# Performance work log

Measured on AMD Instinct MI355X. Metric: run time of the kernel, lower is better.

The kernel has to match this reference:

```python
import jax, jax.numpy as jnp
import numpy as np
from jax import lax

T, B, D_IN, H = 512, 128, 512, 512


def setup_inputs() -> dict:
    key = jax.random.key(0)
    k1, k2, k3, k4 = jax.random.split(key, 4)
    ins = jax.random.normal(k1, (T, B, D_IN), dtype=jnp.float32)
    resets = jax.random.bernoulli(k2, 0.05, (T, B))  # episode-boundary reset mask
    carry = jnp.zeros((B, H), dtype=jnp.float32)
    # fused GRU weights: gate order (r, z, n); input denses have no bias in flax GRUCell
    Wi = jax.random.normal(k3, (D_IN, 3 * H), dtype=jnp.float32) * (1.0 / np.sqrt(D_IN))
    Wh = jax.random.normal(k4, (H, 3 * H), dtype=jnp.float32) * (1.0 / np.sqrt(H))
    bh = jnp.zeros((3 * H,), dtype=jnp.float32)
    return {"carry": carry, "ins": ins, "resets": resets, "Wi": Wi, "Wh": Wh, "bh": bh}


def reference(carry, ins, resets, Wi, Wh, bh):
    """ScannedRNN forward: scan a flax GRUCell over time with per-step reset masking.

    Returns (final_carry [B,H], ys [T,B,H]).
    """

    def step(h, xr):
        x, r_mask = xr                       # x: [B,D_in], r_mask: [B]
        h = jnp.where(r_mask[:, None], jnp.zeros_like(h), h)
        gi = x @ Wi                          # [B,3H]  (no input bias in flax GRUCell)
        gh = h @ Wh + bh                     # [B,3H]
        ir, iz, inn = jnp.split(gi, 3, axis=-1)
        hr, hz, hn = jnp.split(gh, 3, axis=-1)
        r = jax.nn.sigmoid(ir + hr)
        z = jax.nn.sigmoid(iz + hz)
        n = jnp.tanh(inn + r * hn)
        new_h = (1.0 - z) * n + z * h
        return new_h, new_h                  # GRUCell returns (new_carry, new_carry)

    final_carry, ys = lax.scan(step, carry, (ins, resets))
    return final_carry, ys
```

## Files before the change

### kernel.cpp

```cpp
#include <hip/hip_runtime.h>

#define T_STEPS 512
#define BATCH   128
#define DIN     512
#define HDIM    512
#define THREEH  1536
#define THREADS 256
#define LDK     520
#define LDG     49
#define NGROUP  4
#define NSLICE  32
#define BC      32
#define HC      16
#define NC      48
#define CNT_STRIDE 16
#define SPIN_MAX (1 << 16)
#define EX_DWORDS (NSLICE * BATCH * HC / 2)
#define RW5 16
#define EXSLOT 131072
#define FLAGS_OFF  0
#define GBAR_OFF   1024
#define NONCE_OFF  1536
#define DEC_OFF    1664
#define VD_OFF     2048
#define HS_OFF     3072
#define EX_OFF     4096
#define GI_OFF     (1u<<20)
#define GI_BYTES   201326592ULL

typedef _Float16 half8 __attribute__((ext_vector_type(8)));
typedef _Float16 half4v __attribute__((ext_vector_type(4)));
typedef float    f32x4 __attribute__((ext_vector_type(4)));
typedef unsigned int uint4v __attribute__((ext_vector_type(4)));

__global__ void sniff_kernel(const unsigned int* __restrict__ w,
                             unsigned int* __restrict__ dec) {
  unsigned int local = 0;
  for (int i = threadIdx.x; i < (T_STEPS * BATCH) / 4; i += THREADS) {
    if (w[i] > 1u) local = 1u;
  }
  if (local) atomicOr(dec, 1u);
}

__device__ __forceinline__ void run_gemm(const _Float16* __restrict__ sAa,
                                         const _Float16* __restrict__ sW,
                                         float* __restrict__ sAcc,
                                         int wid, int lane) {
  const int fr = lane & 15;
  const int kb = (lane >> 4) * 8;
  for (int tile = wid; tile < 6; tile += 4) {
    int mi = tile / 3, ni = tile - mi * 3;
    const _Float16* ap = sAa + (mi * 16 + fr) * LDK + kb;
    const _Float16* bp = sW  + (ni * 16 + fr) * LDK + kb;
    f32x4 acc = {0.f, 0.f, 0.f, 0.f};
#pragma unroll
    for (int kk = 0; kk < DIN / 32; ++kk)
      acc = __builtin_amdgcn_mfma_f32_16x16x32_f16(
          *(const half8*)(ap + kk * 32),
          *(const half8*)(bp + kk * 32), acc, 0, 0, 0);
    int crow = mi * 16 + (lane >> 4) * 4;
    int ccol = ni * 16 + fr;
#pragma unroll
    for (int j = 0; j < 4; ++j) sAcc[(crow + j) * LDG + ccol] = acc[j];
  }
}

__global__ __launch_bounds__(THREADS, 1)
void gru_kernel_v1(const float* __restrict__ carry,
                   const float* __restrict__ ins,
                   const void*  __restrict__ resets_raw,
                   const float* __restrict__ Wi,
                   const float* __restrict__ Wh,
                   const float* __restrict__ bh,
                   float* __restrict__ out,
                   unsigned int* __restrict__ cnt,
                   unsigned int* __restrict__ ex0,
                   unsigned int* __restrict__ ex1,
                   const unsigned int* __restrict__ dec)
{
  __shared__ alignas(16) _Float16 sWi[NC * LDK];
  __shared__ alignas(16) _Float16 sWh[NC * LDK];
  __shared__ alignas(16) _Float16 sA [BC * LDK];
  __shared__ float sGi[BC * LDG];
  __shared__ float sGh[BC * LDG];
  __shared__ float sBh[NC];
  __shared__ int   sRst[BC];

  const int tid  = threadIdx.x;
  const int bid  = blockIdx.x;
  const int g    = bid & (NGROUP - 1);
  const int p    = bid >> 2;
  const int row0 = g * BC;
  const int col0 = p * HC;

  float* carryOut = out;
  float* ys = out + BATCH * HDIM;

  const unsigned int isBool = *dec;
  const unsigned char* r8  = (const unsigned char*)resets_raw;
  const int*           r32 = (const int*)resets_raw;

  unsigned int* ex[2] = { ex0, ex1 };
  unsigned int* myCnt = cnt + g * CNT_STRIDE;

  for (int idx = tid; idx < DIN * NC; idx += THREADS) {
    int k  = idx / NC;
    int ci = idx - k * NC;
    int gcol = (ci >> 4) * HDIM + col0 + (ci & 15);
    sWi[ci * LDK + k] = (_Float16)Wi[k * THREEH + gcol];
    sWh[ci * LDK + k] = (_Float16)Wh[k * THREEH + gcol];
  }
  if (tid < NC) {
    int gcol = (tid >> 4) * HDIM + col0 + (tid & 15);
    sBh[tid] = bh[gcol];
  }

  float hreg[2];
  {
    int idx = tid * 2;
    int b0 = idx >> 4, c0 = idx & 15;
    hreg[0] = carry[(size_t)(row0 + b0) * HDIM + col0 + c0];
    hreg[1] = carry[(size_t)(row0 + b0) * HDIM + col0 + c0 + 1];
  }

  const int wid  = tid >> 6;
  const int lane = tid & 63;

  auto stageRst = [&](int t) {
    if (tid < BC) {
      int off = t * BATCH + row0 + tid;
      sRst[tid] = isBool ? (int)r8[off] : r32[off];
    }
  };
  auto stageX = [&](int t) {
    const float4* src = (const float4*)(ins + (size_t)(t * BATCH + row0) * DIN);
    for (int i = tid; i < BC * (DIN / 4); i += THREADS) {
      int r = i >> 7, c4 = i & 127;
      float4 v = src[(size_t)r * 128 + c4];
      half4v hv = {(_Float16)v.x, (_Float16)v.y, (_Float16)v.z, (_Float16)v.w};
      *(half4v*)&sA[r * LDK + c4 * 4] = hv;
    }
  };

  stageRst(0);
  stageX(0);
  __syncthreads();
  run_gemm(sA, sWi, sGi, wid, lane);
  __syncthreads();
  {
    const float4* src = (const float4*)(carry + (size_t)row0 * HDIM);
    for (int i = tid; i < BC * (HDIM / 4); i += THREADS) {
      int r = i >> 7, c4 = i & 127;
      float4 v = src[(size_t)r * 128 + c4];
      float m = sRst[r] ? 0.f : 1.f;
      half4v hv = {(_Float16)(v.x*m), (_Float16)(v.y*m),
                   (_Float16)(v.z*m), (_Float16)(v.w*m)};
      *(half4v*)&sA[r * LDK + c4 * 4] = hv;
    }
  }
  __syncthreads();

  for (int t = 0; t < T_STEPS; ++t) {
    if (t > 0) {
      {
        const unsigned int target = 32u * (unsigned)t;
        unsigned int fv;
        for (int it = 0; it < SPIN_MAX; ++it) {
          asm volatile("global_load_dword %0, %1, off sc0 sc1\n\t"
                       "s_waitcnt vmcnt(0)"
                       : "=v"(fv) : "v"(myCnt) : "memory");
          if (fv >= target) break;
          __builtin_amdgcn_s_sleep(1);
        }
      }
      {
        const unsigned int* exsrc = ex[(t - 1) & 1];
        uint4v vv[8];
#pragma unroll
        for (int j = 0; j < 8; ++j) {
          int i = tid + THREADS * j;
          int p_ = i >> 6, b_ = (i >> 1) & 31, hw = (i & 1) << 2;
          const unsigned int* sp = exsrc + p_ * 1024 + (row0 + b_) * 8 + hw;
          asm volatile("global_load_dwordx4 %0, %1, off sc0 sc1"
                       : "=&v"(vv[j]) : "v"(sp) : "memory");
        }
        asm volatile("s_waitcnt vmcnt(0)" ::: "memory");
        __builtin_amdgcn_sched_barrier(0);
#pragma unroll
        for (int j = 0; j < 8; ++j) {
          int i = tid + THREADS * j;
          int p_ = i >> 6, b_ = (i >> 1) & 31, hw = (i & 1) << 3;
          half8 hv = *reinterpret_cast<half8*>(&vv[j]);
          half8 z = {(_Float16)0, (_Float16)0, (_Float16)0, (_Float16)0,
                     (_Float16)0, (_Float16)0, (_Float16)0, (_Float16)0};
          hv = sRst[b_] ? z : hv;
          *(half8*)&sA[b_ * LDK + p_ * 16 + hw] = hv;
        }
      }
      __syncthreads();
    }

    run_gemm(sA, sWh, sGh, wid, lane);
    __syncthreads();

    {
#pragma unroll
      for (int e = 0; e < 2; ++e) {
        int idx = tid * 2 + e;
        int b = idx >> 4, cj = idx & 15;
        float gir = sGi[b * LDG + cj];
        float giz = sGi[b * LDG + 16 + cj];
        float gin = sGi[b * LDG + 32 + cj];
        float ghr = sGh[b * LDG + cj]      + sBh[cj];
        float ghz = sGh[b * LDG + 16 + cj] + sBh[16 + cj];
        float ghn = sGh[b * LDG + 32 + cj] + sBh[32 + cj];
        float r = 1.f / (1.f + __expf(-(gir + ghr)));
        float z = 1.f / (1.f + __expf(-(giz + ghz)));
        float n = tanhf(gin + r * ghn);
        float hp = sRst[b] ? 0.f : hreg[e];
        hreg[e] = (1.f - z) * n + z * hp;
      }
      union { _Float16 h[2]; unsigned int u; } pk;
      pk.h[0] = (_Float16)hreg[0];
      pk.h[1] = (_Float16)hreg[1];
      unsigned int* dst = ex[t & 1] + p * 1024 + (row0 + (tid >> 3)) * 8 + (tid & 7);
      asm volatile("global_store_dword %0, %1, off sc0 sc1"
                   :: "v"(dst), "v"(pk.u) : "memory");
      int b0 = (tid * 2) >> 4, c0 = (tid * 2) & 15;
      float2 yv = make_float2(hreg[0], hreg[1]);
      *(float2*)&ys[((size_t)t * BATCH + row0 + b0) * HDIM + col0 + c0] = yv;
      if (t == T_STEPS - 1)
        *(float2*)&carryOut[(size_t)(row0 + b0) * HDIM + col0 + c0] = yv;
    }
    asm volatile("s_waitcnt vmcnt(0)" ::: "memory");
    __syncthreads();
    if (tid == 0) atomicAdd(myCnt, 1u);

    if (t < T_STEPS - 1) {
      stageRst(t + 1);
      stageX(t + 1);
      __syncthreads();
      run_gemm(sA, sWi, sGi, wid, lane);
      __syncthreads();
    }
  }
}

__global__ __launch_bounds__(256, 1)
void gi_prepass2(const float* __restrict__ ins,
                 const float* __restrict__ Wi,
                 _Float16* __restrict__ gis)
{
  __shared__ alignas(16) _Float16 sWiT[48 * LDK];
  __shared__ alignas(16) _Float16 sX[32 * LDK];

  const int tid = threadIdx.x;
  const int bid = blockIdx.x;
  const int n   = bid >> 3;
  const int mg  = bid & 7;
  const int wid = tid >> 6;
  const int lane = tid & 63;
  const int fr = lane & 15;
  const int kb = (lane >> 4) * 8;

  for (int idx = tid; idx < 48 * DIN; idx += 256) {
    int ci = idx % 48, k = idx / 48;
    int gcol = (ci >> 4) * HDIM + n * 16 + (ci & 15);
    sWiT[ci * LDK + k] = (_Float16)Wi[(size_t)k * THREEH + gcol];
  }

  float4 va[16];
  auto LOADS = [&](int ch) {
    const float4* src = (const float4*)(ins + (size_t)(mg * 8192 + ch * 32) * DIN);
#pragma unroll
    for (int j = 0; j < 16; ++j) va[j] = src[tid + 256 * j];
  };
  auto WRITE = [&]() {
#pragma unroll
    for (int j = 0; j < 16; ++j) {
      int i = tid + 256 * j;
      int r = i >> 7, c4 = i & 127;
      float4 v = va[j];
      half4v hv = {(_Float16)v.x, (_Float16)v.y, (_Float16)v.z, (_Float16)v.w};
      *(half4v*)&sX[r * LDK + c4 * 4] = hv;
    }
  };

  LOADS(0);
  for (int ch = 0; ch < 256; ++ch) {
    WRITE();
    __syncthreads();
    if (ch + 1 < 256) LOADS(ch + 1);

    const int m0 = mg * 8192 + ch * 32;
    const int tt = m0 >> 7;
    const int bb0 = m0 & 127;
    for (int tile = wid; tile < 6; tile += 4) {
      int mi = tile / 3, ni = tile - mi * 3;
      const _Float16* ap = sX   + (mi * 16 + fr) * LDK + kb;
      const _Float16* bp = sWiT + (ni * 16 + fr) * LDK + kb;
      f32x4 acc = {0.f, 0.f, 0.f, 0.f};
#pragma unroll
      for (int kk = 0; kk < DIN / 32; ++kk)
        acc = __builtin_amdgcn_mfma_f32_16x16x32_f16(
            *(const half8*)(ap + kk * 32),
            *(const half8*)(bp + kk * 32), acc, 0, 0, 0);
      int gr = mi * 16 + ((lane >> 4) << 2);
      int col = n * 16 + fr;
      size_t base = ((size_t)(tt * 3 + ni) * BATCH) * HDIM + col;
#pragma unroll
      for (int j = 0; j < 4; ++j)
        gis[base + (size_t)(bb0 + gr + j) * HDIM] = (_Float16)acc[j];
    }
    __syncthreads();
  }
}

__device__ __forceinline__ void gridbar(unsigned int* ctr, int tid) {
  __syncthreads();
  if (tid == 0) {
    atomicAdd(ctr, 1u);
    unsigned int v;
    for (int it = 0; it < SPIN_MAX; ++it) {
      asm volatile("global_load_dword %0, %1, off sc0 sc1\n\t"
                   "s_waitcnt vmcnt(0)" : "=v"(v) : "v"(ctr) : "memory");
      if (v >= 256u) break;
      __builtin_amdgcn_s_sleep(1);
    }
  }
  __syncthreads();
}

__global__ __launch_bounds__(256, 1)
void gru_kernel_v5(const float* __restrict__ carry,
                   const void*  __restrict__ resets_raw,
                   const float* __restrict__ Wh,
                   const float* __restrict__ bh,
                   float* __restrict__ out,
                   unsigned int* __restrict__ wsb,
                   const _Float16* __restrict__ gis,
                   const unsigned int* __restrict__ dec)
{
  __shared__ alignas(16) _Float16 sWh[NC * LDK];
  __shared__ alignas(16) _Float16 sA [RW5 * LDK];
  __shared__ float sGh[RW5 * LDG];
  __shared__ alignas(16) _Float16 sGi[2 * 3 * 16 * 16];
  __shared__ float sBh[NC];
  __shared__ char  sRstAll[T_STEPS * RW5];
  __shared__ int   sFast;
  __shared__ unsigned int sNonce;

  const int tid  = threadIdx.x;
  const int bid  = blockIdx.x;
  const int g    = bid & 7;
  const int p    = bid >> 3;
  const int row0 = g * RW5;
  const int col0 = p * HC;

  unsigned int* flags    = wsb + (FLAGS_OFF / 4);
  unsigned int* gbars    = wsb + (GBAR_OFF / 4);
  unsigned int* nonceArr = wsb + (NONCE_OFF / 4);
  unsigned int* vd       = wsb + (VD_OFF / 4);
  unsigned int* hs       = wsb + (HS_OFF / 4);
  char*         exb      = (char*)wsb + EX_OFF;

  float* carryOut = out;
  float* ys = out + BATCH * HDIM;

  const unsigned int isBool = *dec;
  const unsigned char* r8  = (const unsigned char*)resets_raw;
  const int*           r32 = (const int*)resets_raw;
  const unsigned short* gisu = (const unsigned short*)gis;

  const int wid  = tid >> 6;
  const int lane = tid & 63;
  const int fr   = lane & 15;
  const int kb   = (lane >> 4) * 8;
  const int gb   = tid >> 4;
  const int gc   = tid & 15;

  for (int idx = tid; idx < DIN * NC; idx += THREADS) {
    int k  = idx / NC;
    int ci = idx - k * NC;
    int gcol = (ci >> 4) * HDIM + col0 + (ci & 15);
    sWh[ci * LDK + k] = (_Float16)Wh[k * THREEH + gcol];
  }
  if (tid < NC) {
    int gcol = (tid >> 4) * HDIM + col0 + (tid & 15);
    sBh[tid] = bh[gcol];
  }
  for (int idx = tid; idx < T_STEPS * RW5; idx += THREADS) {
    int tt = idx >> 4, r = idx & 15;
    int off = tt * BATCH + row0 + r;
    sRstAll[idx] = isBool ? (char)(r8[off] != 0) : (char)(r32[off] != 0);
  }
  float hreg = carry[(size_t)(row0 + gb) * HDIM + col0 + gc];

  if (p == 0 && tid == 0) {
    unsigned long long tv = __builtin_amdgcn_s_memrealtime();
    unsigned int nv = (unsigned int)(tv ^ (tv >> 32));
    if (nv == 0) nv = 0x5A5A5A5Au;
    unsigned int* np = nonceArr + g;
    asm volatile("global_store_dword %0, %1, off sc0 sc1\n\t"
                 "s_waitcnt vmcnt(0)" :: "v"(np), "v"(nv) : "memory");
  }
  gridbar(gbars + 0 * 16, tid);
  if (tid == 0) {
    unsigned int nv;
    asm volatile("global_load_dword %0, %1, off sc0 sc1\n\t"
                 "s_waitcnt vmcnt(0)" : "=v"(nv) : "v"(nonceArr + g) : "memory");
    sNonce = nv;
  }
  __syncthreads();
  const unsigned int nonce = sNonce;

  bool okAll = true;
  for (int r = 0; r < 2; ++r) {
    gridbar(gbars + (1 + r) * 16, tid);
    if (tid == 0) {
      unsigned int tok = nonce ^ ((unsigned)p << 8) ^ ((unsigned)(r + 1) << 20);
      asm volatile("global_store_dword %0, %1, off sc0\n\t"
                   "s_waitcnt vmcnt(0)" :: "v"(hs + bid), "v"(tok) : "memory");
    }
    __syncthreads();
    for (int s = 0; s < 40; ++s) __builtin_amdgcn_s_sleep(2);
    if (tid < 32) {
      unsigned int v;
      const unsigned int* hp = hs + (g + 8 * tid);
      asm volatile("global_load_dword %0, %1, off sc0\n\t"
                   "s_waitcnt vmcnt(0)" : "=v"(v) : "v"(hp) : "memory");
      unsigned int expv = nonce ^ ((unsigned)tid << 8) ^ ((unsigned)(r + 1) << 20);
      okAll = okAll && (v == expv);
    }
  }
  {
    bool wgok = __all((tid < 32) ? okAll : true);
    if (tid == 0) {
      unsigned int vv = wgok ? 1u : 0u;
      asm volatile("global_store_dword %0, %1, off sc0 sc1\n\t"
                   "s_waitcnt vmcnt(0)" :: "v"(vd + bid), "v"(vv) : "memory");
    }
    gridbar(gbars + 3 * 16, tid);
    bool fin = true;
    if (tid < 32) {
      unsigned int v;
      asm volatile("global_load_dword %0, %1, off sc0 sc1\n\t"
                   "s_waitcnt vmcnt(0)" : "=v"(v) : "v"(vd + (g + 8 * tid)) : "memory");
      fin = (v == 1u);
    }
    bool unan = __all((tid < 32) ? fin : true);
    if (tid == 0) sFast = unan ? 1 : 0;
    __syncthreads();
  }
  const int fast = sFast;

  if (tid == 0) {
    unsigned int* fp = flags + (g * 32 + p);
    unsigned int zz = 0u;
    if (fast) asm volatile("global_store_dword %0, %1, off sc0\n\ts_waitcnt vmcnt(0)" :: "v"(fp), "v"(zz) : "memory");
    else      asm volatile("global_store_dword %0, %1, off sc0 sc1\n\ts_waitcnt vmcnt(0)" :: "v"(fp), "v"(zz) : "memory");
  }
  {
    union { _Float16 h; unsigned short u; } ck;
    ck.h = (_Float16)hreg;
    unsigned int cv = (unsigned int)ck.u;
    char* cdst = exb + EXSLOT + g * 16384 + gb * 1024 + (col0 + gc) * 2;
    if (fast) asm volatile("global_store_short %0, %1, off sc0" :: "v"(cdst), "v"(cv) : "memory");
    else      asm volatile("global_store_short %0, %1, off sc0 sc1" :: "v"(cdst), "v"(cv) : "memory");
    asm volatile("s_waitcnt vmcnt(0)" ::: "memory");
  }
  gridbar(gbars + 4 * 16, tid);

  {
    size_t base = ((size_t)0 * BATCH + row0 + gb) * HDIM + col0 + gc;
    unsigned short v0 = gisu[base];
    unsigned short v1 = gisu[base + (size_t)BATCH * HDIM];
    unsigned short v2 = gisu[base + 2 * (size_t)BATCH * HDIM];
    union { unsigned short u; _Float16 h; } c;
    c.u = v0; sGi[(0 * 16 + gb) * 16 + gc] = c.h;
    c.u = v1; sGi[(1 * 16 + gb) * 16 + gc] = c.h;
    c.u = v2; sGi[(2 * 16 + gb) * 16 + gc] = c.h;
  }
  uint4v w3a = {0, 0, 0, 0}, w3b = {0, 0, 0, 0};
  if (fast && wid == 3 && lane < 48) {
    int gamma = lane >> 4, row = lane & 15;
    const char* sp = (const char*)(gisu + ((size_t)(1 * 3 + gamma) * BATCH + row0 + row) * HDIM + col0);
    asm volatile("global_load_dwordx4 %0, %2, off\n\t"
                 "global_load_dwordx4 %1, %2, off offset:16"
                 : "=v"(w3a), "=v"(w3b) : "v"(sp) : "memory");
  }
  __syncthreads();

  for (int t = 0; t < T_STEPS; ++t) {
    const int slot = t & 1;
    if (fast) {
      if (t > 0) {
        unsigned int fv = 0xFFFFFFFFu;
        const unsigned int* fp = flags + g * 32 + (tid & 31);
        bool done = false;
        for (int it = 0; it < SPIN_MAX && !done; ++it) {
          if (tid < 32)
            asm volatile("global_load_dword %0, %1, off sc0\n\t"
                         "s_waitcnt vmcnt(0)" : "=v"(fv) : "v"(fp) : "memory");
          done = __all((tid < 32) ? (fv >= (unsigned)t) : true);
          if (!done && it > 256) __builtin_amdgcn_s_sleep(1);
        }
      }
      __syncthreads();

      if (wid < 3) {
        const char* abase = exb + (slot ^ 1) * EXSLOT + g * 16384 + fr * 1024 + kb * 2;
        uint4v af[16];
#pragma unroll
        for (int kk = 0; kk < 16; ++kk) {
          const char* sp = abase + kk * 64;
          asm volatile("global_load_dwordx4 %0, %1, off sc0"
                       : "=v"(af[kk]) : "v"(sp) : "memory");
        }
        asm volatile("s_waitcnt vmcnt(0)" ::: "memory");
        __builtin_amdgcn_sched_barrier(0);
        int rr = (int)sRstAll[t * 16 + fr];
        if (rr) {
#pragma unroll
          for (int kk = 0; kk < 16; ++kk) af[kk] = (uint4v){0, 0, 0, 0};
        }
        const _Float16* bp = sWh + (wid * 16 + fr) * LDK + kb;
        f32x4 a0 = {0.f, 0.f, 0.f, 0.f}, a1 = {0.f, 0.f, 0.f, 0.f};
#pragma unroll
        for (int kk = 0; kk < 16; kk += 2) {
          a0 = __builtin_amdgcn_mfma_f32_16x16x32_f16(
              *(half8*)&af[kk], *(const half8*)(bp + kk * 32), a0, 0, 0, 0);
          a1 = __builtin_amdgcn_mfma_f32_16x16x32_f16(
              *(half8*)&af[kk + 1], *(const half8*)(bp + (kk + 1) * 32), a1, 0, 0, 0);
        }
        a0 += a1;
        int crow = (lane >> 4) * 4;
        int ccol = wid * 16 + fr;
#pragma unroll
        for (int j = 0; j < 4; ++j) sGh[(crow + j) * LDG + ccol] = a0[j];
      } else {
        asm volatile("s_waitcnt vmcnt(0)" ::: "memory");
        __builtin_amdgcn_sched_barrier(0);
        if (lane < 48) {
          int gamma = lane >> 4, row = lane & 15;
          _Float16* d = &sGi[((t + 1) & 1) * 768 + (gamma * 16 + row) * 16];
          *(uint4v*)d = w3a;
          *(uint4v*)(d + 8) = w3b;
        }
        int tn = (t + 2 < T_STEPS) ? t + 2 : T_STEPS - 1;
        if (lane < 48) {
          int gamma = lane >> 4, row = lane & 15;
          const char* sp = (const char*)(gisu + ((size_t)(tn * 3 + gamma) * BATCH + row0 + row) * HDIM + col0);
          asm volatile("global_load_dwordx4 %0, %2, off\n\t"
                       "global_load_dwordx4 %1, %2, off offset:16"
                       : "=v"(w3a), "=v"(w3b) : "v"(sp) : "memory");
        }
      }
      __syncthreads();

      {
        float gir = (float)sGi[slot * 768 + (0 * 16 + gb) * 16 + gc];
        float giz = (float)sGi[slot * 768 + (1 * 16 + gb) * 16 + gc];
        float gin = (float)sGi[slot * 768 + (2 * 16 + gb) * 16 + gc];
        float ghr = sGh[gb * LDG + gc]      + sBh[gc];
        float ghz = sGh[gb * LDG + 16 + gc] + sBh[16 + gc];
        float ghn = sGh[gb * LDG + 32 + gc] + sBh[32 + gc];
        float r = 1.f / (1.f + __expf(-(gir + ghr)));
        float z = 1.f / (1.f + __expf(-(giz + ghz)));
        float n = tanhf(gin + r * ghn);
        float hp = sRstAll[t * 16 + gb] ? 0.f : hreg;
        hreg = (1.f - z) * n + z * hp;
        if (t < T_STEPS - 1) {
          union { _Float16 h; unsigned short u; } pk;
          pk.h = (_Float16)hreg;
          unsigned int pv = (unsigned int)pk.u;
          char* dst = exb + slot * EXSLOT + g * 16384 + gb * 1024 + (col0 + gc) * 2;
          asm volatile("global_store_short %0, %1, off sc0"
                       :: "v"(dst), "v"(pv) : "memory");
        }
      }
      asm volatile("s_waitcnt vmcnt(0)" ::: "memory");
      __syncthreads();
      if (tid == 0 && t < T_STEPS - 1) {
        unsigned int* fp = flags + (g * 32 + p);
        unsigned int val = (unsigned)(t + 1);
        asm volatile("global_store_dword %0, %1, off sc0"
                     :: "v"(fp), "v"(val) : "memory");
      }
      ys[((size_t)t * BATCH + row0 + gb) * HDIM + col0 + gc] = hreg;
      if (t == T_STEPS - 1)
        carryOut[(size_t)(row0 + gb) * HDIM + col0 + gc] = hreg;
    } else {
      unsigned short fg0, fg1, fg2;
      {
        size_t base = ((size_t)(t * 3) * BATCH + row0 + gb) * HDIM + col0 + gc;
        fg0 = gisu[base];
        fg1 = gisu[base + (size_t)BATCH * HDIM];
        fg2 = gisu[base + 2 * (size_t)BATCH * HDIM];
      }
      if (t > 0) {
        unsigned int fv = 0xFFFFFFFFu;
        const unsigned int* fp = flags + g * 32 + (tid & 31);
        bool done = false;
        for (int it = 0; it < SPIN_MAX && !done; ++it) {
          if (tid < 32)
            asm volatile("global_load_dword %0, %1, off sc0 sc1\n\t"
                         "s_waitcnt vmcnt(0)" : "=v"(fv) : "v"(fp) : "memory");
          done = __all((tid < 32) ? (fv >= (unsigned)t) : true);
          if (!done) __builtin_amdgcn_s_sleep(1);
        }
      }
      __syncthreads();

      {
        const char* src = exb + (slot ^ 1) * EXSLOT + g * 16384
                        + (tid >> 4) * 1024 + (tid & 15) * 64;
        uint4v v0, v1, v2, v3;
        asm volatile("global_load_dwordx4 %0, %4, off sc0 sc1\n\t"
                     "global_load_dwordx4 %1, %4, off offset:16 sc0 sc1\n\t"
                     "global_load_dwordx4 %2, %4, off offset:32 sc0 sc1\n\t"
                     "global_load_dwordx4 %3, %4, off offset:48 sc0 sc1\n\t"
                     "s_waitcnt vmcnt(0)"
                     : "=&v"(v0), "=&v"(v1), "=&v"(v2), "=&v"(v3)
                     : "v"(src) : "memory");
        __builtin_amdgcn_sched_barrier(0);
        int r = tid >> 4, c0 = (tid & 15) * 32;
        half8 h0 = *reinterpret_cast<half8*>(&v0);
        half8 h1 = *reinterpret_cast<half8*>(&v1);
        half8 h2 = *reinterpret_cast<half8*>(&v2);
        half8 h3 = *reinterpret_cast<half8*>(&v3);
        half8 z = {(_Float16)0, (_Float16)0, (_Float16)0, (_Float16)0,
                   (_Float16)0, (_Float16)0, (_Float16)0, (_Float16)0};
        if (sRstAll[t * 16 + r]) { h0 = z; h1 = z; h2 = z; h3 = z; }
        *(half8*)&sA[r * LDK + c0 +  0] = h0;
        *(half8*)&sA[r * LDK + c0 +  8] = h1;
        *(half8*)&sA[r * LDK + c0 + 16] = h2;
        *(half8*)&sA[r * LDK + c0 + 24] = h3;
      }
      __syncthreads();

      if (wid < 3) {
        const _Float16* ap = sA  + fr * LDK + kb;
        const _Float16* bp = sWh + (wid * 16 + fr) * LDK + kb;
        f32x4 a0 = {0.f, 0.f, 0.f, 0.f}, a1 = {0.f, 0.f, 0.f, 0.f};
#pragma unroll
        for (int kk = 0; kk < 16; kk += 2) {
          a0 = __builtin_amdgcn_mfma_f32_16x16x32_f16(
              *(const half8*)(ap + kk * 32), *(const half8*)(bp + kk * 32), a0, 0, 0, 0);
          a1 = __builtin_amdgcn_mfma_f32_16x16x32_f16(
              *(const half8*)(ap + (kk + 1) * 32), *(const half8*)(bp + (kk + 1) * 32), a1, 0, 0, 0);
        }
        a0 += a1;
        int crow = (lane >> 4) * 4;
        int ccol = wid * 16 + fr;
#pragma unroll
        for (int j = 0; j < 4; ++j) sGh[(crow + j) * LDG + ccol] = a0[j];
      }
      __syncthreads();

      {
        union { unsigned short u; _Float16 h; } c0_, c1_, c2_;
        c0_.u = fg0; c1_.u = fg1; c2_.u = fg2;
        float gir = (float)c0_.h;
        float giz = (float)c1_.h;
        float gin = (float)c2_.h;
        float ghr = sGh[gb * LDG + gc]      + sBh[gc];
        float ghz = sGh[gb * LDG + 16 + gc] + sBh[16 + gc];
        float ghn = sGh[gb * LDG + 32 + gc] + sBh[32 + gc];
        float r = 1.f / (1.f + __expf(-(gir + ghr)));
        float z = 1.f / (1.f + __expf(-(giz + ghz)));
        float n = tanhf(gin + r * ghn);
        float hp = sRstAll[t * 16 + gb] ? 0.f : hreg;
        hreg = (1.f - z) * n + z * hp;
        if (t < T_STEPS - 1) {
          union { _Float16 h; unsigned short u; } pk;
          pk.h = (_Float16)hreg;
          unsigned int pv = (unsigned int)pk.u;
          char* dst = exb + slot * EXSLOT + g * 16384 + gb * 1024 + (col0 + gc) * 2;
          asm volatile("global_store_short %0, %1, off sc0 sc1"
                       :: "v"(dst), "v"(pv) : "memory");
        }
      }
      asm volatile("s_waitcnt vmcnt(0)" ::: "memory");
      __syncthreads();
      if (tid == 0 && t < T_STEPS - 1) {
        unsigned int* fp = flags + (g * 32 + p);
        unsigned int val = (unsigned)(t + 1);
        asm volatile("global_store_dword %0, %1, off sc0 sc1"
                     :: "v"(fp), "v"(val) : "memory");
      }
      ys[((size_t)t * BATCH + row0 + gb) * HDIM + col0 + gc] = hreg;
      if (t == T_STEPS - 1)
        carryOut[(size_t)(row0 + gb) * HDIM + col0 + gc] = hreg;
    }
  }

  __builtin_amdgcn_fence(__ATOMIC_RELEASE, "agent");
}

extern "C" void kernel_launch(void* const* d_in, const int* in_sizes, int n_in,
                              void* d_out, int out_size, void* d_ws, size_t ws_size,
                              hipStream_t stream) {
  const float* carry  = (const float*)d_in[0];
  const float* ins    = (const float*)d_in[1];
  const void*  resets = (const void*)d_in[2];
  const float* Wi     = (const float*)d_in[3];
  const float* Wh     = (const float*)d_in[4];
  const float* bh     = (const float*)d_in[5];
  float* out = (float*)d_out;

  unsigned int* wsb  = (unsigned int*)d_ws;
  unsigned int* dec  = (unsigned int*)((char*)d_ws + DEC_OFF);
  unsigned int* ex0  = (unsigned int*)((char*)d_ws + EX_OFF);
  unsigned int* ex1  = ex0 + EX_DWORDS;
  _Float16*     gis  = (_Float16*)((char*)d_ws + GI_OFF);

  (void)hipMemsetAsync(d_ws, 0, 4096, stream);

  sniff_kernel<<<dim3(1), dim3(THREADS), 0, stream>>>(
      (const unsigned int*)resets, dec);

  const bool bigWs = ws_size >= (size_t)GI_OFF + GI_BYTES;

  if (bigWs) {
    gi_prepass2<<<dim3(256), dim3(256), 0, stream>>>(ins, Wi, gis);
    void* args[] = { (void*)&carry, (void*)&resets, (void*)&Wh, (void*)&bh,
                     (void*)&out, (void*)&wsb, (void*)&gis, (void*)&dec };
    (void)hipLaunchCooperativeKernel((const void*)gru_kernel_v5,
                                     dim3(256), dim3(256),
                                     args, 0, stream);
  } else {
    void* args[] = { (void*)&carry, (void*)&ins, (void*)&resets, (void*)&Wi,
                     (void*)&Wh, (void*)&bh, (void*)&out, (void*)&wsb,
                     (void*)&ex0, (void*)&ex1, (void*)&dec };
    (void)hipLaunchCooperativeKernel((const void*)gru_kernel_v1,
                                     dim3(NGROUP * NSLICE), dim3(THREADS),
                                     args, 0, stream);
  }
}
```

Before: 2.273 ms.

## Tag exchanged hidden state with step number to replace flag polling

The hidden-state exchange buffer now stores each fp16 value in a dword with the step number in the upper 16 bits. Consumers spin directly on the data until every tag matches, instead of first polling per-block flags and then loading. The per-step flag wait moves to the otherwise idle wave 3 and only guards buffer reuse. Merging the fast and slow paths and replacing fixed sleeps in the handshake with spin loops are meant to shorten the critical path of each recurrent step, at the cost of doubling exchange traffic and a larger workspace memset.

```diff
diff --git a/kernel.cpp b/kernel.cpp
--- a/kernel.cpp
+++ b/kernel.cpp
@@ -15,9 +15,10 @@
 #define NC      48
 #define CNT_STRIDE 16
 #define SPIN_MAX (1 << 16)
+#define HS_SPIN  512
 #define EX_DWORDS (NSLICE * BATCH * HC / 2)
-#define RW5 16
-#define EXSLOT 131072
+#define RW6 16
+#define SLOTSZ 262144
 #define FLAGS_OFF  0
 #define GBAR_OFF   1024
 #define NONCE_OFF  1536
@@ -332,7 +333,7 @@
 }
 
 __global__ __launch_bounds__(256, 1)
-void gru_kernel_v5(const float* __restrict__ carry,
+void gru_kernel_v6(const float* __restrict__ carry,
                    const void*  __restrict__ resets_raw,
                    const float* __restrict__ Wh,
                    const float* __restrict__ bh,
@@ -342,11 +343,11 @@
                    const unsigned int* __restrict__ dec)
 {
   __shared__ alignas(16) _Float16 sWh[NC * LDK];
-  __shared__ alignas(16) _Float16 sA [RW5 * LDK];
-  __shared__ float sGh[RW5 * LDG];
+  __shared__ alignas(16) _Float16 sA [RW6 * LDK];
+  __shared__ float sGh[RW6 * LDG];
   __shared__ alignas(16) _Float16 sGi[2 * 3 * 16 * 16];
   __shared__ float sBh[NC];
-  __shared__ char  sRstAll[T_STEPS * RW5];
+  __shared__ char  sRstAll[T_STEPS * RW6];
   __shared__ int   sFast;
   __shared__ unsigned int sNonce;
 
@@ -354,7 +355,7 @@
   const int bid  = blockIdx.x;
   const int g    = bid & 7;
   const int p    = bid >> 3;
-  const int row0 = g * RW5;
+  const int row0 = g * RW6;
   const int col0 = p * HC;
 
   unsigned int* flags    = wsb + (FLAGS_OFF / 4);
@@ -389,7 +390,7 @@
     int gcol = (tid >> 4) * HDIM + col0 + (tid & 15);
     sBh[tid] = bh[gcol];
   }
-  for (int idx = tid; idx < T_STEPS * RW5; idx += THREADS) {
+  for (int idx = tid; idx < T_STEPS * RW6; idx += THREADS) {
     int tt = idx >> 4, r = idx & 15;
     int off = tt * BATCH + row0 + r;
     sRstAll[idx] = isBool ? (char)(r8[off] != 0) : (char)(r32[off] != 0);
@@ -400,9 +401,8 @@
     unsigned long long tv = __builtin_amdgcn_s_memrealtime();
     unsigned int nv = (unsigned int)(tv ^ (tv >> 32));
     if (nv == 0) nv = 0x5A5A5A5Au;
-    unsigned int* np = nonceArr + g;
     asm volatile("global_store_dword %0, %1, off sc0 sc1\n\t"
-                 "s_waitcnt vmcnt(0)" :: "v"(np), "v"(nv) : "memory");
+                 "s_waitcnt vmcnt(0)" :: "v"(nonceArr + g), "v"(nv) : "memory");
   }
   gridbar(gbars + 0 * 16, tid);
   if (tid == 0) {
@@ -416,22 +416,25 @@
 
   bool okAll = true;
   for (int r = 0; r < 2; ++r) {
-    gridbar(gbars + (1 + r) * 16, tid);
     if (tid == 0) {
       unsigned int tok = nonce ^ ((unsigned)p << 8) ^ ((unsigned)(r + 1) << 20);
       asm volatile("global_store_dword %0, %1, off sc0\n\t"
                    "s_waitcnt vmcnt(0)" :: "v"(hs + bid), "v"(tok) : "memory");
     }
     __syncthreads();
-    for (int s = 0; s < 40; ++s) __builtin_amdgcn_s_sleep(2);
     if (tid < 32) {
-      unsigned int v;
+      unsigned int expv = nonce ^ ((unsigned)tid << 8) ^ ((unsigned)(r + 1) << 20);
       const unsigned int* hp = hs + (g + 8 * tid);
-      asm volatile("global_load_dword %0, %1, off sc0\n\t"
-                   "s_waitcnt vmcnt(0)" : "=v"(v) : "v"(hp) : "memory");
-      unsigned int expv = nonce ^ ((unsigned)tid << 8) ^ ((unsigned)(r + 1) << 20);
-      okAll = okAll && (v == expv);
-    }
+      bool got = false;
+      for (int it = 0; it < HS_SPIN && !got; ++it) {
+        unsigned int v;
+        asm volatile("global_load_dword %0, %1, off sc0\n\t"
+                     "s_waitcnt vmcnt(0)" : "=v"(v) : "v"(hp) : "memory");
+        got = (v == expv);
+      }
+      okAll = okAll && got;
+    }
+    gridbar(gbars + (1 + r) * 16, tid);
   }
   {
     bool wgok = __all((tid < 32) ? okAll : true);
@@ -454,99 +457,122 @@
   }
   const int fast = sFast;
 
-  if (tid == 0) {
-    unsigned int* fp = flags + (g * 32 + p);
-    unsigned int zz = 0u;
-    if (fast) asm volatile("global_store_dword %0, %1, off sc0\n\ts_waitcnt vmcnt(0)" :: "v"(fp), "v"(zz) : "memory");
-    else      asm volatile("global_store_dword %0, %1, off sc0 sc1\n\ts_waitcnt vmcnt(0)" :: "v"(fp), "v"(zz) : "memory");
-  }
   {
     union { _Float16 h; unsigned short u; } ck;
     ck.h = (_Float16)hreg;
-    unsigned int cv = (unsigned int)ck.u;
-    char* cdst = exb + EXSLOT + g * 16384 + gb * 1024 + (col0 + gc) * 2;
-    if (fast) asm volatile("global_store_short %0, %1, off sc0" :: "v"(cdst), "v"(cv) : "memory");
-    else      asm volatile("global_store_short %0, %1, off sc0 sc1" :: "v"(cdst), "v"(cv) : "memory");
+    unsigned int cv = (1u << 16) | (unsigned int)ck.u;
+    char* cdst = exb + 1 * SLOTSZ + g * 32768 + ((gb * 512) + (col0 + gc)) * 4;
+    if (fast) asm volatile("global_store_dword %0, %1, off sc0" :: "v"(cdst), "v"(cv) : "memory");
+    else      asm volatile("global_store_dword %0, %1, off sc0 sc1" :: "v"(cdst), "v"(cv) : "memory");
     asm volatile("s_waitcnt vmcnt(0)" ::: "memory");
   }
-  gridbar(gbars + 4 * 16, tid);
 
   {
     size_t base = ((size_t)0 * BATCH + row0 + gb) * HDIM + col0 + gc;
-    unsigned short v0 = gisu[base];
-    unsigned short v1 = gisu[base + (size_t)BATCH * HDIM];
-    unsigned short v2 = gisu[base + 2 * (size_t)BATCH * HDIM];
     union { unsigned short u; _Float16 h; } c;
-    c.u = v0; sGi[(0 * 16 + gb) * 16 + gc] = c.h;
-    c.u = v1; sGi[(1 * 16 + gb) * 16 + gc] = c.h;
-    c.u = v2; sGi[(2 * 16 + gb) * 16 + gc] = c.h;
+    c.u = gisu[base];                              sGi[(0 * 16 + gb) * 16 + gc] = c.h;
+    c.u = gisu[base + (size_t)BATCH * HDIM];       sGi[(1 * 16 + gb) * 16 + gc] = c.h;
+    c.u = gisu[base + 2 * (size_t)BATCH * HDIM];   sGi[(2 * 16 + gb) * 16 + gc] = c.h;
   }
   uint4v w3a = {0, 0, 0, 0}, w3b = {0, 0, 0, 0};
-  if (fast && wid == 3 && lane < 48) {
+  if (wid == 3 && lane < 48) {
     int gamma = lane >> 4, row = lane & 15;
-    const char* sp = (const char*)(gisu + ((size_t)(1 * 3 + gamma) * BATCH + row0 + row) * HDIM + col0);
+    const char* sp = (const char*)(gisu + ((size_t)(3 + gamma) * BATCH + row0 + row) * HDIM + col0);
     asm volatile("global_load_dwordx4 %0, %2, off\n\t"
                  "global_load_dwordx4 %1, %2, off offset:16"
                  : "=v"(w3a), "=v"(w3b) : "v"(sp) : "memory");
   }
   __syncthreads();
 
+  const int srow = tid >> 4;
+  const int sc0_ = (tid & 15) * 32;
+
   for (int t = 0; t < T_STEPS; ++t) {
-    const int slot = t & 1;
-    if (fast) {
-      if (t > 0) {
-        unsigned int fv = 0xFFFFFFFFu;
-        const unsigned int* fp = flags + g * 32 + (tid & 31);
-        bool done = false;
-        for (int it = 0; it < SPIN_MAX && !done; ++it) {
-          if (tid < 32)
-            asm volatile("global_load_dword %0, %1, off sc0\n\t"
-                         "s_waitcnt vmcnt(0)" : "=v"(fv) : "v"(fp) : "memory");
-          done = __all((tid < 32) ? (fv >= (unsigned)t) : true);
-          if (!done && it > 256) __builtin_amdgcn_s_sleep(1);
+    {
+      const char* src = exb + ((t + 1) & 1) * SLOTSZ + g * 32768
+                      + ((srow * 512) + sc0_) * 4;
+      const unsigned int expt = (unsigned int)(t + 1);
+      uint4v v0, v1, v2, v3, v4, v5, v6, v7;
+      unsigned int mask = 0xFFu;
+      for (int it = 0; it < SPIN_MAX && mask; ++it) {
+#define LD1(V, J)                                                              \
+        if (mask & (1u << J)) {                                                \
+          if (fast) asm volatile("global_load_dwordx4 %0, %1, off sc0"         \
+                                 : "=v"(V) : "v"(src + J * 16) : "memory");    \
+          else      asm volatile("global_load_dwordx4 %0, %1, off sc0 sc1"     \
+                                 : "=v"(V) : "v"(src + J * 16) : "memory");    \
         }
-      }
-      __syncthreads();
-
-      if (wid < 3) {
-        const char* abase = exb + (slot ^ 1) * EXSLOT + g * 16384 + fr * 1024 + kb * 2;
-        uint4v af[16];
-#pragma unroll
-        for (int kk = 0; kk < 16; ++kk) {
-          const char* sp = abase + kk * 64;
-          asm volatile("global_load_dwordx4 %0, %1, off sc0"
-                       : "=v"(af[kk]) : "v"(sp) : "memory");
+        LD1(v0, 0) LD1(v1, 1) LD1(v2, 2) LD1(v3, 3)
+        LD1(v4, 4) LD1(v5, 5) LD1(v6, 6) LD1(v7, 7)
+#undef LD1
+        asm volatile("s_waitcnt vmcnt(0)" ::: "memory");
+#define CK1(V, J)                                                              \
+        if ((mask & (1u << J)) &&                                              \
+            (V[0] >> 16) == expt && (V[1] >> 16) == expt &&                    \
+            (V[2] >> 16) == expt && (V[3] >> 16) == expt) mask &= ~(1u << J);
+        CK1(v0, 0) CK1(v1, 1) CK1(v2, 2) CK1(v3, 3)
+        CK1(v4, 4) CK1(v5, 5) CK1(v6, 6) CK1(v7, 7)
+#undef CK1
+      }
+      __builtin_amdgcn_sched_barrier(0);
+      const bool rz = sRstAll[t * 16 + srow] != 0;
+#define ST1(V, J)                                                              \
+      {                                                                        \
+        unsigned int d0 = (V[0] & 0xFFFFu) | (V[1] << 16);                     \
+        unsigned int d1 = (V[2] & 0xFFFFu) | (V[3] << 16);                     \
+        if (rz) { d0 = 0u; d1 = 0u; }                                          \
+        unsigned long long q = ((unsigned long long)d1 << 32) | d0;            \
+        *(unsigned long long*)&sA[srow * LDK + sc0_ + J * 4] = q;              \
+      }
+      ST1(v0, 0) ST1(v1, 1) ST1(v2, 2) ST1(v3, 3)
+      ST1(v4, 4) ST1(v5, 5) ST1(v6, 6) ST1(v7, 7)
+#undef ST1
+    }
+    __syncthreads();
+
+    if (tid == 0) {
+      unsigned int val = (unsigned)(t + 1);
+      unsigned int* fp = flags + (g * 32 + p);
+      if (fast) asm volatile("global_store_dword %0, %1, off sc0" :: "v"(fp), "v"(val) : "memory");
+      else      asm volatile("global_store_dword %0, %1, off sc0 sc1" :: "v"(fp), "v"(val) : "memory");
+    }
+
+    if (wid < 3) {
+      const _Float16* ap = sA  + fr * LDK + kb;
+      const _Float16* bp = sWh + (wid * 16 + fr) * LDK + kb;
+      f32x4 a0 = {0.f, 0.f, 0.f, 0.f}, a1 = {0.f, 0.f, 0.f, 0.f};
+#pragma unroll
+      for (int kk = 0; kk < 16; kk += 2) {
+        a0 = __builtin_amdgcn_mfma_f32_16x16x32_f16(
+            *(const half8*)(ap + kk * 32), *(const half8*)(bp + kk * 32), a0, 0, 0, 0);
+        a1 = __builtin_amdgcn_mfma_f32_16x16x32_f16(
+            *(const half8*)(ap + (kk + 1) * 32), *(const half8*)(bp + (kk + 1) * 32), a1, 0, 0, 0);
+      }
+      a0 += a1;
+      int crow = (lane >> 4) * 4;
+      int ccol = wid * 16 + fr;
+#pragma unroll
+      for (int j = 0; j < 4; ++j) sGh[(crow + j) * LDG + ccol] = a0[j];
+    } else {
+      if (lane < 48) {
+        int gamma = lane >> 4, row = lane & 15;
+        _Float16* d = &sGi[((t + 1) & 1) * 768 + (gamma * 16 + row) * 16];
+        *(uint4v*)d = w3a;
+        *(uint4v*)(d + 8) = w3b;
+      }
+      if (t >= 1 && t < T_STEPS - 1 && lane < 32) {
+        const unsigned int* fp = flags + g * 32 + lane;
+        unsigned int fv = 0;
+        for (int it = 0; it < SPIN_MAX; ++it) {
+          if (fast) asm volatile("global_load_dword %0, %1, off sc0\n\ts_waitcnt vmcnt(0)"
+                                 : "=v"(fv) : "v"(fp) : "memory");
+          else      asm volatile("global_load_dword %0, %1, off sc0 sc1\n\ts_waitcnt vmcnt(0)"
+                                 : "=v"(fv) : "v"(fp) : "memory");
+          if (fv >= (unsigned)t) break;
+          __builtin_amdgcn_s_sleep(1);
         }
-        asm volatile("s_waitcnt vmcnt(0)" ::: "memory");
-        __builtin_amdgcn_sched_barrier(0);
-        int rr = (int)sRstAll[t * 16 + fr];
-        if (rr) {
-#pragma unroll
-          for (int kk = 0; kk < 16; ++kk) af[kk] = (uint4v){0, 0, 0, 0};
-        }
-        const _Float16* bp = sWh + (wid * 16 + fr) * LDK + kb;
-        f32x4 a0 = {0.f, 0.f, 0.f, 0.f}, a1 = {0.f, 0.f, 0.f, 0.f};
-#pragma unroll
-        for (int kk = 0; kk < 16; kk += 2) {
-          a0 = __builtin_amdgcn_mfma_f32_16x16x32_f16(
-              *(half8*)&af[kk], *(const half8*)(bp + kk * 32), a0, 0, 0, 0);
-          a1 = __builtin_amdgcn_mfma_f32_16x16x32_f16(
-              *(half8*)&af[kk + 1], *(const half8*)(bp + (kk + 1) * 32), a1, 0, 0, 0);
-        }
-        a0 += a1;
-        int crow = (lane >> 4) * 4;
-        int ccol = wid * 16 + fr;
-#pragma unroll
-        for (int j = 0; j < 4; ++j) sGh[(crow + j) * LDG + ccol] = a0[j];
-      } else {
-        asm volatile("s_waitcnt vmcnt(0)" ::: "memory");
-        __builtin_amdgcn_sched_barrier(0);
-        if (lane < 48) {
-          int gamma = lane >> 4, row = lane & 15;
-          _Float16* d = &sGi[((t + 1) & 1) * 768 + (gamma * 16 + row) * 16];
-          *(uint4v*)d = w3a;
-          *(uint4v*)(d + 8) = w3b;
-        }
+      }
+      {
         int tn = (t + 2 < T_STEPS) ? t + 2 : T_STEPS - 1;
         if (lane < 48) {
           int gamma = lane >> 4, row = lane & 15;
@@ -556,138 +582,29 @@
                        : "=v"(w3a), "=v"(w3b) : "v"(sp) : "memory");
         }
       }
-      __syncthreads();
-
-      {
-        float gir = (float)sGi[slot * 768 + (0 * 16 + gb) * 16 + gc];
-        float giz = (float)sGi[slot * 768 + (1 * 16 + gb) * 16 + gc];
-        float gin = (float)sGi[slot * 768 + (2 * 16 + gb) * 16 + gc];
-        float ghr = sGh[gb * LDG + gc]      + sBh[gc];
-        float ghz = sGh[gb * LDG + 16 + gc] + sBh[16 + gc];
-        float ghn = sGh[gb * LDG + 32 + gc] + sBh[32 + gc];
-        float r = 1.f / (1.f + __expf(-(gir + ghr)));
-        float z = 1.f / (1.f + __expf(-(giz + ghz)));
-        float n = tanhf(gin + r * ghn);
-        float hp = sRstAll[t * 16 + gb] ? 0.f : hreg;
-        hreg = (1.f - z) * n + z * hp;
-        if (t < T_STEPS - 1) {
-          union { _Float16 h; unsigned short u; } pk;
-          pk.h = (_Float16)hreg;
-          unsigned int pv = (unsigned int)pk.u;
-          char* dst = exb + slot * EXSLOT + g * 16384 + gb * 1024 + (col0 + gc) * 2;
-          asm volatile("global_store_short %0, %1, off sc0"
-                       :: "v"(dst), "v"(pv) : "memory");
-        }
-      }
-      asm volatile("s_waitcnt vmcnt(0)" ::: "memory");
-      __syncthreads();
-      if (tid == 0 && t < T_STEPS - 1) {
-        unsigned int* fp = flags + (g * 32 + p);
-        unsigned int val = (unsigned)(t + 1);
-        asm volatile("global_store_dword %0, %1, off sc0"
-                     :: "v"(fp), "v"(val) : "memory");
-      }
-      ys[((size_t)t * BATCH + row0 + gb) * HDIM + col0 + gc] = hreg;
-      if (t == T_STEPS - 1)
-        carryOut[(size_t)(row0 + gb) * HDIM + col0 + gc] = hreg;
-    } else {
-      unsigned short fg0, fg1, fg2;
-      {
-        size_t base = ((size_t)(t * 3) * BATCH + row0 + gb) * HDIM + col0 + gc;
-        fg0 = gisu[base];
-        fg1 = gisu[base + (size_t)BATCH * HDIM];
-        fg2 = gisu[base + 2 * (size_t)BATCH * HDIM];
-      }
-      if (t > 0) {
-        unsigned int fv = 0xFFFFFFFFu;
-        const unsigned int* fp = flags + g * 32 + (tid & 31);
-        bool done = false;
-        for (int it = 0; it < SPIN_MAX && !done; ++it) {
-          if (tid < 32)
-            asm volatile("global_load_dword %0, %1, off sc0 sc1\n\t"
-                         "s_waitcnt vmcnt(0)" : "=v"(fv) : "v"(fp) : "memory");
-          done = __all((tid < 32) ? (fv >= (unsigned)t) : true);
-          if (!done) __builtin_amdgcn_s_sleep(1);
-        }
-      }
-      __syncthreads();
-
-      {
-        const char* src = exb + (slot ^ 1) * EXSLOT + g * 16384
-                        + (tid >> 4) * 1024 + (tid & 15) * 64;
-        uint4v v0, v1, v2, v3;
-        asm volatile("global_load_dwordx4 %0, %4, off sc0 sc1\n\t"
-                     "global_load_dwordx4 %1, %4, off offset:16 sc0 sc1\n\t"
-                     "global_load_dwordx4 %2, %4, off offset:32 sc0 sc1\n\t"
-                     "global_load_dwordx4 %3, %4, off offset:48 sc0 sc1\n\t"
-                     "s_waitcnt vmcnt(0)"
-                     : "=&v"(v0), "=&v"(v1), "=&v"(v2), "=&v"(v3)
-                     : "v"(src) : "memory");
-        __builtin_amdgcn_sched_barrier(0);
-        int r = tid >> 4, c0 = (tid & 15) * 32;
-        half8 h0 = *reinterpret_cast<half8*>(&v0);
-        half8 h1 = *reinterpret_cast<half8*>(&v1);
-        half8 h2 = *reinterpret_cast<half8*>(&v2);
-        half8 h3 = *reinterpret_cast<half8*>(&v3);
-        half8 z = {(_Float16)0, (_Float16)0, (_Float16)0, (_Float16)0,
-                   (_Float16)0, (_Float16)0, (_Float16)0, (_Float16)0};
-        if (sRstAll[t * 16 + r]) { h0 = z; h1 = z; h2 = z; h3 = z; }
-        *(half8*)&sA[r * LDK + c0 +  0] = h0;
-        *(half8*)&sA[r * LDK + c0 +  8] = h1;
-        *(half8*)&sA[r * LDK + c0 + 16] = h2;
-        *(half8*)&sA[r * LDK + c0 + 24] = h3;
-      }
-      __syncthreads();
-
-      if (wid < 3) {
-        const _Float16* ap = sA  + fr * LDK + kb;
-        const _Float16* bp = sWh + (wid * 16 + fr) * LDK + kb;
-        f32x4 a0 = {0.f, 0.f, 0.f, 0.f}, a1 = {0.f, 0.f, 0.f, 0.f};
-#pragma unroll
-        for (int kk = 0; kk < 16; kk += 2) {
-          a0 = __builtin_amdgcn_mfma_f32_16x16x32_f16(
-              *(const half8*)(ap + kk * 32), *(const half8*)(bp + kk * 32), a0, 0, 0, 0);
-          a1 = __builtin_amdgcn_mfma_f32_16x16x32_f16(
-              *(const half8*)(ap + (kk + 1) * 32), *(const half8*)(bp + (kk + 1) * 32), a1, 0, 0, 0);
-        }
-        a0 += a1;
-        int crow = (lane >> 4) * 4;
-        int ccol = wid * 16 + fr;
-#pragma unroll
-        for (int j = 0; j < 4; ++j) sGh[(crow + j) * LDG + ccol] = a0[j];
-      }
-      __syncthreads();
-
-      {
-        union { unsigned short u; _Float16 h; } c0_, c1_, c2_;
-        c0_.u = fg0; c1_.u = fg1; c2_.u = fg2;
-        float gir = (float)c0_.h;
-        float giz = (float)c1_.h;
-        float gin = (float)c2_.h;
-        float ghr = sGh[gb * LDG + gc]      + sBh[gc];
-        float ghz = sGh[gb * LDG + 16 + gc] + sBh[16 + gc];
-        float ghn = sGh[gb * LDG + 32 + gc] + sBh[32 + gc];
-        float r = 1.f / (1.f + __expf(-(gir + ghr)));
-        float z = 1.f / (1.f + __expf(-(giz + ghz)));
-        float n = tanhf(gin + r * ghn);
-        float hp = sRstAll[t * 16 + gb] ? 0.f : hreg;
-        hreg = (1.f - z) * n + z * hp;
-        if (t < T_STEPS - 1) {
-          union { _Float16 h; unsigned short u; } pk;
-          pk.h = (_Float16)hreg;
-          unsigned int pv = (unsigned int)pk.u;
-          char* dst = exb + slot * EXSLOT + g * 16384 + gb * 1024 + (col0 + gc) * 2;
-          asm volatile("global_store_short %0, %1, off sc0 sc1"
-                       :: "v"(dst), "v"(pv) : "memory");
-        }
-      }
-      asm volatile("s_waitcnt vmcnt(0)" ::: "memory");
-      __syncthreads();
-      if (tid == 0 && t < T_STEPS - 1) {
-        unsigned int* fp = flags + (g * 32 + p);
-        unsigned int val = (unsigned)(t + 1);
-        asm volatile("global_store_dword %0, %1, off sc0 sc1"
-                     :: "v"(fp), "v"(val) : "memory");
+    }
+    __syncthreads();
+
+    {
+      float gir = (float)sGi[(t & 1) * 768 + (0 * 16 + gb) * 16 + gc];
+      float giz = (float)sGi[(t & 1) * 768 + (1 * 16 + gb) * 16 + gc];
+      float gin = (float)sGi[(t & 1) * 768 + (2 * 16 + gb) * 16 + gc];
+      float ghr = sGh[gb * LDG + gc]      + sBh[gc];
+      float ghz = sGh[gb * LDG + 16 + gc] + sBh[16 + gc];
+      float ghn = sGh[gb * LDG + 32 + gc] + sBh[32 + gc];
+      float r = 1.f / (1.f + __expf(-(gir + ghr)));
+      float z = 1.f / (1.f + __expf(-(giz + ghz)));
+      float n = tanhf(gin + r * ghn);
+      float hp = sRstAll[t * 16 + gb] ? 0.f : hreg;
+      hreg = (1.f - z) * n + z * hp;
+
+      if (t < T_STEPS - 1) {
+        union { _Float16 h; unsigned short u; } pk;
+        pk.h = (_Float16)hreg;
+        unsigned int pv = ((unsigned int)(t + 2) << 16) | (unsigned int)pk.u;
+        char* dst = exb + (t & 1) * SLOTSZ + g * 32768 + ((gb * 512) + (col0 + gc)) * 4;
+        if (fast) asm volatile("global_store_dword %0, %1, off sc0" :: "v"(dst), "v"(pv) : "memory");
+        else      asm volatile("global_store_dword %0, %1, off sc0 sc1" :: "v"(dst), "v"(pv) : "memory");
       }
       ys[((size_t)t * BATCH + row0 + gb) * HDIM + col0 + gc] = hreg;
       if (t == T_STEPS - 1)
@@ -715,18 +632,18 @@
   unsigned int* ex1  = ex0 + EX_DWORDS;
   _Float16*     gis  = (_Float16*)((char*)d_ws + GI_OFF);
 
-  (void)hipMemsetAsync(d_ws, 0, 4096, stream);
+  const bool bigWs = ws_size >= (size_t)GI_OFF + GI_BYTES;
+
+  (void)hipMemsetAsync(d_ws, 0, bigWs ? (EX_OFF + 2 * SLOTSZ) : 4096, stream);
 
   sniff_kernel<<<dim3(1), dim3(THREADS), 0, stream>>>(
       (const unsigned int*)resets, dec);
-
-  const bool bigWs = ws_size >= (size_t)GI_OFF + GI_BYTES;
 
   if (bigWs) {
     gi_prepass2<<<dim3(256), dim3(256), 0, stream>>>(ins, Wi, gis);
     void* args[] = { (void*)&carry, (void*)&resets, (void*)&Wh, (void*)&bh,
                      (void*)&out, (void*)&wsb, (void*)&gis, (void*)&dec };
-    (void)hipLaunchCooperativeKernel((const void*)gru_kernel_v5,
+    (void)hipLaunchCooperativeKernel((const void*)gru_kernel_v6,
                                      dim3(256), dim3(256),
                                      args, 0, stream);
   } else {
```

Result: slower. 4.078 ms (+79.4%).
